# Optimization experiments

Hardware: AMD Instinct MI355X
Metric: run time of the kernel (lower is better)

Reference implementation:

```python
import jax, jax.numpy as jnp
import numpy as np

B, S, D, H, DK, DV = 4, 2048, 512, 8, 64, 64


def setup_inputs() -> dict:
    key0 = jax.random.key(0)
    ks = jax.random.split(key0, 11)
    w = 0.02
    return {
        "query": jax.random.normal(ks[0], (B, S, D), dtype=jnp.float32),
        "key": jax.random.normal(ks[1], (B, S, D), dtype=jnp.float32),
        "value": jax.random.normal(ks[2], (B, S, D), dtype=jnp.float32),
        "Wq": jax.random.normal(ks[3], (D, DK), dtype=jnp.float32) * w,
        "bq": jnp.zeros((DK,), dtype=jnp.float32),
        "Wk": jax.random.normal(ks[4], (D, DK), dtype=jnp.float32) * w,
        "bk": jnp.zeros((DK,), dtype=jnp.float32),
        "Wv": jax.random.normal(ks[5], (D, DV), dtype=jnp.float32) * w,
        "bv": jnp.zeros((DV,), dtype=jnp.float32),
        "Wo": jax.random.normal(ks[6], (H * DV, D), dtype=jnp.float32) * w,
        "bo": jnp.zeros((D,), dtype=jnp.float32),
    }


def reference(query, key, value, Wq, bq, Wk, bk, Wv, bv, Wo, bo):
    # NOTE: original module applies the SAME Dense layers to every head
    # (q_list = [self.query(query) for _ in range(heads)]), so all H heads
    # are mathematically identical -> compute one head and replicate.
    # NOTE: V is projected from `key`, not `value` (faithful to source bug).
    q = query @ Wq + bq          # [B, S, DK]
    k = key @ Wk + bk            # [B, S, DK]
    v = key @ Wv + bv            # [B, S, DV]
    scale = np.sqrt(DK).astype(np.float32)
    scores = jnp.einsum("bqd,bkd->bqk", q, k) / scale  # [B, S, S]
    # masked_mha=True and training=True -> causal mask, fill -1e19
    causal = jnp.triu(jnp.ones((S, S), dtype=scores.dtype), 1)
    scores = scores + causal * jnp.asarray(-1e19, scores.dtype)
    attn = jax.nn.softmax(scores, axis=-1)              # [B, S, S]
    o = jnp.einsum("bqk,bkv->bqv", attn, v)             # [B, S, DV]
    # concat of H identical heads along last axis == tile
    concat = jnp.tile(o, (1, 1, H))                     # [B, S, H*DV]
    return concat @ Wo + bo                             # [B, S, D]
```

## Files before the change

kernel.cpp:

```cpp
#include <hip/hip_runtime.h>
#include <hip/hip_bf16.h>


#define BB 4
#define SS 2048
#define BS (BB*SS)
#define MSHIFT 8.0f

typedef __bf16 v8bf __attribute__((ext_vector_type(8)));
typedef __bf16 v4bf __attribute__((ext_vector_type(4)));
typedef float  v4f  __attribute__((ext_vector_type(4)));

__device__ inline v8bf cvt8(float4 f0, float4 f1) {
    v8bf r;
    r[0] = (__bf16)f0.x; r[1] = (__bf16)f0.y; r[2] = (__bf16)f0.z; r[3] = (__bf16)f0.w;
    r[4] = (__bf16)f1.x; r[5] = (__bf16)f1.y; r[6] = (__bf16)f1.z; r[7] = (__bf16)f1.w;
    return r;
}

__global__ __launch_bounds__(512) void prep_kernel(
    const float* __restrict__ Wq, const float* __restrict__ bq,
    const float* __restrict__ Wk, const float* __restrict__ bk,
    const float* __restrict__ Wv, const float* __restrict__ bv,
    const float* __restrict__ Wo,
    __bf16* __restrict__ Wt, float* __restrict__ bs,
    __bf16* __restrict__ WoEt)
{
    const int t = threadIdx.x, y = blockIdx.y;
    const int idx = blockIdx.x * 512 + t;
    if (y < 3) {
        const float* W  = (y == 0) ? Wq : (y == 1) ? Wk : Wv;
        const float* bb = (y == 0) ? bq : (y == 1) ? bk : bv;
        const float s = (y == 0) ? (0.125f * 1.44269504088896340736f) : 1.0f;
        int c = idx & 63, k = idx >> 6;
        Wt[y * 32768 + c * 512 + k] = (__bf16)(W[k * 64 + c] * s);
        if (blockIdx.x == 0 && t < 64) bs[y * 64 + t] = bb[t] * s;
    } else {
        int d = idx & 511, k = idx >> 9;
        float sum = 0.f;
#pragma unroll
        for (int h = 0; h < 8; h++) sum += Wo[(size_t)(h * 64 + k) * 512 + d];
        WoEt[d * 64 + k] = (__bf16)sum;
    }
}

__global__ __launch_bounds__(256) void proj_kernel(
    const float* __restrict__ query, const float* __restrict__ key,
    const __bf16* __restrict__ Wt, const float* __restrict__ bs,
    __bf16* __restrict__ Qp, __bf16* __restrict__ Kp, __bf16* __restrict__ Vt)
{
    const int t = threadIdx.x;
    const int gw = (blockIdx.x * 256 + t) >> 6;
    const int lane = t & 63, lq = lane & 15, quad = lane >> 4;
    const int kind = gw >> 11;
    const int rr  = gw & 2047;
    const int rows = (rr >> 2) * 16;
    const int cb   = (rr & 3) * 16;
    const float* arow = ((kind == 0) ? query : key) + (size_t)(rows + lq) * 512;

    if (kind == 0) {
        const __bf16* W = Wt + (cb + lq) * 512;
        const float bb = bs[cb + lq];
        v4f acc = {bb, bb, bb, bb};
#pragma unroll 4
        for (int k0 = 0; k0 < 512; k0 += 32) {
            float4 f0 = *(const float4*)(arow + k0 + quad * 8);
            float4 f1 = *(const float4*)(arow + k0 + quad * 8 + 4);
            v8bf a = cvt8(f0, f1);
            v8bf b = *(const v8bf*)(W + k0 + quad * 8);
            acc = __builtin_amdgcn_mfma_f32_16x16x32_bf16(a, b, acc, 0, 0, 0);
        }
#pragma unroll
        for (int r = 0; r < 4; r++)
            Qp[(size_t)(rows + quad * 4 + r) * 64 + cb + lq] = (__bf16)acc[r];
    } else {
        const __bf16* Wk_ = Wt + 32768  + (cb + lq) * 512;
        const __bf16* Wv_ = Wt + 65536  + (cb + lq) * 512;
        const float bk_ = bs[64 + cb + lq], bv_ = bs[128 + cb + lq];
        v4f ak = {bk_, bk_, bk_, bk_}, av = {bv_, bv_, bv_, bv_};
#pragma unroll 4
        for (int k0 = 0; k0 < 512; k0 += 32) {
            float4 f0 = *(const float4*)(arow + k0 + quad * 8);
            float4 f1 = *(const float4*)(arow + k0 + quad * 8 + 4);
            v8bf a  = cvt8(f0, f1);
            v8bf b0 = *(const v8bf*)(Wk_ + k0 + quad * 8);
            v8bf b1 = *(const v8bf*)(Wv_ + k0 + quad * 8);
            ak = __builtin_amdgcn_mfma_f32_16x16x32_bf16(a, b0, ak, 0, 0, 0);
            av = __builtin_amdgcn_mfma_f32_16x16x32_bf16(a, b1, av, 0, 0, 0);
        }
#pragma unroll
        for (int r = 0; r < 4; r++)
            Kp[(size_t)(rows + quad * 4 + r) * 64 + cb + lq] = (__bf16)ak[r];
        v4bf o4; o4[0] = (__bf16)av[0]; o4[1] = (__bf16)av[1];
        o4[2] = (__bf16)av[2]; o4[3] = (__bf16)av[3];
        *(v4bf*)&Vt[(size_t)(cb + lq) * BS + rows + quad * 4] = o4;
    }
}

__global__ __launch_bounds__(256) void attn_kernel(
    const __bf16* __restrict__ Qp,
    const __bf16* __restrict__ Kp,
    const __bf16* __restrict__ Vt,
    __bf16* __restrict__ Opart,
    float* __restrict__ lpart,
    int nch)
{
    __shared__ __bf16 Ks[64][72];
    __shared__ __bf16 Vs[64][72];
    __shared__ __bf16 Ps[4][16][72];

    const int t    = threadIdx.x;
    const int lane = t & 63;
    const int w    = t >> 6;
    const int b    = blockIdx.x & 3;
    const int qt   = 31 - (blockIdx.x >> 2);
    const int c    = blockIdx.y;
    const int qbase = qt * 64;
    const int L    = qbase + 64;
    const int cs   = ((L + nch * 64 - 1) / (nch * 64)) * 64;
    const int klo  = c * cs;
    const int khi  = min(klo + cs, L);
    const size_t bbase = (size_t)b * SS;

    const int lq   = lane & 15;
    const int quad = lane >> 4;
    const int qrow_w = qbase + w * 16;
    const int wmax   = qrow_w + 15;

    const size_t qoff = (bbase + qrow_w + lq) * 64;
    v8bf qa0 = *(const v8bf*)(Qp + qoff + quad * 8);
    v8bf qa1 = *(const v8bf*)(Qp + qoff + 32 + quad * 8);

    v8bf ones;
#pragma unroll
    for (int i = 0; i < 8; i++) ones[i] = (__bf16)1.0f;

    v4f o[4] = {};
    v4f lacc = {};

    const int ky0 = t >> 3,         dd0 = (t & 7) * 8;
    const int ky1 = (t + 256) >> 3, dd1 = dd0;

    v8bf kpre0, kpre1, vpre0, vpre1;
    if (klo < khi) {
        kpre0 = *(const v8bf*)(Kp + (bbase + klo + ky0) * 64 + dd0);
        kpre1 = *(const v8bf*)(Kp + (bbase + klo + ky1) * 64 + dd1);
        vpre0 = *(const v8bf*)(Vt + (size_t)ky0 * BS + bbase + klo + dd0);
        vpre1 = *(const v8bf*)(Vt + (size_t)ky1 * BS + bbase + klo + dd1);
    }

    for (int kb = klo; kb < khi; kb += 64) {
        __syncthreads();
        *(v8bf*)&Ks[ky0][dd0] = kpre0;
        *(v8bf*)&Ks[ky1][dd1] = kpre1;
        *(v8bf*)&Vs[ky0][dd0] = vpre0;
        *(v8bf*)&Vs[ky1][dd1] = vpre1;
        if (kb + 64 < khi) {
            kpre0 = *(const v8bf*)(Kp + (bbase + kb + 64 + ky0) * 64 + dd0);
            kpre1 = *(const v8bf*)(Kp + (bbase + kb + 64 + ky1) * 64 + dd1);
            vpre0 = *(const v8bf*)(Vt + (size_t)ky0 * BS + bbase + kb + 64 + dd0);
            vpre1 = *(const v8bf*)(Vt + (size_t)ky1 * BS + bbase + kb + 64 + dd1);
        }
        __syncthreads();
        if (kb > wmax) continue;

        v4f s[4];
#pragma unroll
        for (int n = 0; n < 4; n++) {
            v8bf ka  = *(const v8bf*)&Ks[n * 16 + lq][quad * 8];
            v8bf kb2 = *(const v8bf*)&Ks[n * 16 + lq][32 + quad * 8];
            v4f z = {0.f, 0.f, 0.f, 0.f};
            z    = __builtin_amdgcn_mfma_f32_16x16x32_bf16(qa0, ka,  z, 0, 0, 0);
            s[n] = __builtin_amdgcn_mfma_f32_16x16x32_bf16(qa1, kb2, z, 0, 0, 0);
        }

        const int row0 = qrow_w + quad * 4;
        const int col0 = kb + lq;
#pragma unroll
        for (int n = 0; n < 4; n++)
#pragma unroll
            for (int r = 0; r < 4; r++) {
                float e = exp2f(s[n][r] - MSHIFT);
                e = (col0 + n * 16 > row0 + r) ? 0.f : e;
                Ps[w][quad * 4 + r][n * 16 + lq] = (__bf16)e;
            }
        v8bf pa0 = *(const v8bf*)&Ps[w][lq][quad * 8];
        v8bf pa1 = *(const v8bf*)&Ps[w][lq][32 + quad * 8];

        lacc = __builtin_amdgcn_mfma_f32_16x16x32_bf16(pa0, ones, lacc, 0, 0, 0);
        lacc = __builtin_amdgcn_mfma_f32_16x16x32_bf16(pa1, ones, lacc, 0, 0, 0);

#pragma unroll
        for (int vt = 0; vt < 4; vt++) {
            v8bf vb0 = *(const v8bf*)&Vs[vt * 16 + lq][quad * 8];
            v8bf vb1 = *(const v8bf*)&Vs[vt * 16 + lq][32 + quad * 8];
            o[vt] = __builtin_amdgcn_mfma_f32_16x16x32_bf16(pa0, vb0, o[vt], 0, 0, 0);
            o[vt] = __builtin_amdgcn_mfma_f32_16x16x32_bf16(pa1, vb1, o[vt], 0, 0, 0);
        }
    }

#pragma unroll
    for (int vt = 0; vt < 4; vt++)
#pragma unroll
        for (int r = 0; r < 4; r++) {
            int qrow = qrow_w + quad * 4 + r;
            Opart[((size_t)c * BS + bbase + qrow) * 64 + vt * 16 + lq] = (__bf16)o[vt][r];
        }
    if (lq < 4) {
        int qrow = qrow_w + quad * 4 + lq;
        lpart[(size_t)c * BS + bbase + qrow] = lacc[lq];
    }
}

__global__ __launch_bounds__(256) void outmerge_kernel(
    const __bf16* __restrict__ Opart, const float* __restrict__ lpart,
    const __bf16* __restrict__ WoEt, const float* __restrict__ bo,
    float* __restrict__ out, int nch)
{
    __shared__ __bf16 Os[16][72];
    const int t = threadIdx.x;
    const int rows0 = blockIdx.x * 16;
    {
        int row = t >> 4, d0 = (t & 15) * 4;
        float den = 0.f;
        for (int c = 0; c < nch; c++) den += lpart[(size_t)c * BS + rows0 + row];
        const float inv = 1.f / den;
        float a0 = 0.f, a1 = 0.f, a2 = 0.f, a3 = 0.f;
        for (int c = 0; c < nch; c++) {
            v4bf v = *(const v4bf*)&Opart[((size_t)c * BS + rows0 + row) * 64 + d0];
            a0 += (float)v[0]; a1 += (float)v[1]; a2 += (float)v[2]; a3 += (float)v[3];
        }
        Os[row][d0] = (__bf16)(a0 * inv); Os[row][d0 + 1] = (__bf16)(a1 * inv);
        Os[row][d0 + 2] = (__bf16)(a2 * inv); Os[row][d0 + 3] = (__bf16)(a3 * inv);
    }
    __syncthreads();

    const int lane = t & 63, lq = lane & 15, quad = lane >> 4;
    const int w = t >> 6;
    v8bf a0 = *(const v8bf*)&Os[lq][quad * 8];
    v8bf a1 = *(const v8bf*)&Os[lq][32 + quad * 8];
#pragma unroll
    for (int i = 0; i < 8; i++) {
        const int cb = (w * 8 + i) * 16;
        v8bf b0 = *(const v8bf*)(WoEt + (size_t)(cb + lq) * 64 + quad * 8);
        v8bf b1 = *(const v8bf*)(WoEt + (size_t)(cb + lq) * 64 + 32 + quad * 8);
        const float bb = bo[cb + lq];
        v4f acc = {bb, bb, bb, bb};
        acc = __builtin_amdgcn_mfma_f32_16x16x32_bf16(a0, b0, acc, 0, 0, 0);
        acc = __builtin_amdgcn_mfma_f32_16x16x32_bf16(a1, b1, acc, 0, 0, 0);
#pragma unroll
        for (int r = 0; r < 4; r++)
            out[(size_t)(rows0 + quad * 4 + r) * 512 + cb + lq] = acc[r];
    }
}

extern "C" void kernel_launch(void* const* d_in, const int* in_sizes, int n_in,
                              void* d_out, int out_size, void* d_ws, size_t ws_size,
                              hipStream_t stream) {
    const float* query = (const float*)d_in[0];
    const float* key   = (const float*)d_in[1];
    const float* Wq = (const float*)d_in[3];
    const float* bq = (const float*)d_in[4];
    const float* Wk = (const float*)d_in[5];
    const float* bk = (const float*)d_in[6];
    const float* Wv = (const float*)d_in[7];
    const float* bv = (const float*)d_in[8];
    const float* Wo = (const float*)d_in[9];
    const float* bo = (const float*)d_in[10];
    float* out = (float*)d_out;

    const int nch = (ws_size >= (size_t)12 * 1024 * 1024) ? 8 : 4;

    char* p = (char*)d_ws;
    __bf16* Qp    = (__bf16*)p; p += (size_t)BS * 64 * 2;
    __bf16* Kp    = (__bf16*)p; p += (size_t)BS * 64 * 2;
    __bf16* Vtg   = (__bf16*)p; p += (size_t)BS * 64 * 2;
    __bf16* Opart = (__bf16*)p; p += (size_t)nch * BS * 64 * 2;
    float* lpart = (float*)p;  p += (size_t)nch * BS * 4;
    __bf16* WoEt = (__bf16*)p; p += (size_t)64 * 512 * 2;
    __bf16* Wt   = (__bf16*)p; p += (size_t)3 * 64 * 512 * 2;
    float* bs    = (float*)p;  p += (size_t)3 * 64 * 4;

    prep_kernel<<<dim3(64, 4), 512, 0, stream>>>(Wq, bq, Wk, bk, Wv, bv, Wo, Wt, bs, WoEt);
    proj_kernel<<<1024, 256, 0, stream>>>(query, key, Wt, bs, Qp, Kp, Vtg);
    attn_kernel<<<dim3(128, nch), 256, 0, stream>>>(Qp, Kp, Vtg, Opart, lpart, nch);
    outmerge_kernel<<<512, 256, 0, stream>>>(Opart, lpart, WoEt, bo, out, nch);
}
```

Baseline: 150.2 us.

## Fuse all four kernels into one cooperative persistent kernel with grid syncs

Merges weight prep, QKV projection, chunked causal attention and output merge/projection into a single cooperative launch of 512 blocks, using grid-wide syncs between phases. Each block handles two attention chunks in sequence, and NCH is now fixed at 8. The aim is to remove three kernel launch gaps and the tail idle time between them. In exchange it adds grid.sync overhead, caps occupancy at 2 blocks per CU, and drops the fallback that used fewer chunks when the workspace is small.

Measured after the change: 463.4 us. 3.09x slower.

```diff
diff --git a/kernel.cpp b/kernel.cpp
--- a/kernel.cpp
+++ b/kernel.cpp
@@ -1,11 +1,16 @@
 #include <hip/hip_runtime.h>
 #include <hip/hip_bf16.h>
+#include <hip/hip_cooperative_groups.h>
+
+namespace cg = cooperative_groups;
 
 
 #define BB 4
 #define SS 2048
 #define BS (BB*SS)
+#define NCH 8
 #define MSHIFT 8.0f
+#define QSCALE (0.125f * 1.44269504088896340736f)
 
 typedef __bf16 v8bf __attribute__((ext_vector_type(8)));
 typedef __bf16 v4bf __attribute__((ext_vector_type(4)));
@@ -18,239 +23,250 @@
     return r;
 }
 
-__global__ __launch_bounds__(512) void prep_kernel(
+__global__ __launch_bounds__(256, 2) void fused_kernel(
+    const float* __restrict__ query, const float* __restrict__ key,
     const float* __restrict__ Wq, const float* __restrict__ bq,
     const float* __restrict__ Wk, const float* __restrict__ bk,
     const float* __restrict__ Wv, const float* __restrict__ bv,
-    const float* __restrict__ Wo,
-    __bf16* __restrict__ Wt, float* __restrict__ bs,
+    const float* __restrict__ Wo, const float* __restrict__ bo,
+    float* __restrict__ out,
+    __bf16* __restrict__ Qp,
+    __bf16* __restrict__ Kp,
+    __bf16* __restrict__ Vt,
+    __bf16* __restrict__ Opart,
+    float* __restrict__ lpart,
+    __bf16* __restrict__ Wt,
+    float* __restrict__ bs,
     __bf16* __restrict__ WoEt)
 {
-    const int t = threadIdx.x, y = blockIdx.y;
-    const int idx = blockIdx.x * 512 + t;
-    if (y < 3) {
-        const float* W  = (y == 0) ? Wq : (y == 1) ? Wk : Wv;
-        const float* bb = (y == 0) ? bq : (y == 1) ? bk : bv;
-        const float s = (y == 0) ? (0.125f * 1.44269504088896340736f) : 1.0f;
-        int c = idx & 63, k = idx >> 6;
-        Wt[y * 32768 + c * 512 + k] = (__bf16)(W[k * 64 + c] * s);
-        if (blockIdx.x == 0 && t < 64) bs[y * 64 + t] = bb[t] * s;
-    } else {
-        int d = idx & 511, k = idx >> 9;
-        float sum = 0.f;
-#pragma unroll
-        for (int h = 0; h < 8; h++) sum += Wo[(size_t)(h * 64 + k) * 512 + d];
-        WoEt[d * 64 + k] = (__bf16)sum;
-    }
-}
-
-__global__ __launch_bounds__(256) void proj_kernel(
-    const float* __restrict__ query, const float* __restrict__ key,
-    const __bf16* __restrict__ Wt, const float* __restrict__ bs,
-    __bf16* __restrict__ Qp, __bf16* __restrict__ Kp, __bf16* __restrict__ Vt)
-{
-    const int t = threadIdx.x;
-    const int gw = (blockIdx.x * 256 + t) >> 6;
-    const int lane = t & 63, lq = lane & 15, quad = lane >> 4;
-    const int kind = gw >> 11;
-    const int rr  = gw & 2047;
-    const int rows = (rr >> 2) * 16;
-    const int cb   = (rr & 3) * 16;
-    const float* arow = ((kind == 0) ? query : key) + (size_t)(rows + lq) * 512;
-
-    if (kind == 0) {
-        const __bf16* W = Wt + (cb + lq) * 512;
-        const float bb = bs[cb + lq];
-        v4f acc = {bb, bb, bb, bb};
-#pragma unroll 4
-        for (int k0 = 0; k0 < 512; k0 += 32) {
-            float4 f0 = *(const float4*)(arow + k0 + quad * 8);
-            float4 f1 = *(const float4*)(arow + k0 + quad * 8 + 4);
-            v8bf a = cvt8(f0, f1);
-            v8bf b = *(const v8bf*)(W + k0 + quad * 8);
-            acc = __builtin_amdgcn_mfma_f32_16x16x32_bf16(a, b, acc, 0, 0, 0);
-        }
-#pragma unroll
-        for (int r = 0; r < 4; r++)
-            Qp[(size_t)(rows + quad * 4 + r) * 64 + cb + lq] = (__bf16)acc[r];
-    } else {
-        const __bf16* Wk_ = Wt + 32768  + (cb + lq) * 512;
-        const __bf16* Wv_ = Wt + 65536  + (cb + lq) * 512;
-        const float bk_ = bs[64 + cb + lq], bv_ = bs[128 + cb + lq];
-        v4f ak = {bk_, bk_, bk_, bk_}, av = {bv_, bv_, bv_, bv_};
-#pragma unroll 4
-        for (int k0 = 0; k0 < 512; k0 += 32) {
-            float4 f0 = *(const float4*)(arow + k0 + quad * 8);
-            float4 f1 = *(const float4*)(arow + k0 + quad * 8 + 4);
-            v8bf a  = cvt8(f0, f1);
-            v8bf b0 = *(const v8bf*)(Wk_ + k0 + quad * 8);
-            v8bf b1 = *(const v8bf*)(Wv_ + k0 + quad * 8);
-            ak = __builtin_amdgcn_mfma_f32_16x16x32_bf16(a, b0, ak, 0, 0, 0);
-            av = __builtin_amdgcn_mfma_f32_16x16x32_bf16(a, b1, av, 0, 0, 0);
-        }
-#pragma unroll
-        for (int r = 0; r < 4; r++)
-            Kp[(size_t)(rows + quad * 4 + r) * 64 + cb + lq] = (__bf16)ak[r];
-        v4bf o4; o4[0] = (__bf16)av[0]; o4[1] = (__bf16)av[1];
-        o4[2] = (__bf16)av[2]; o4[3] = (__bf16)av[3];
-        *(v4bf*)&Vt[(size_t)(cb + lq) * BS + rows + quad * 4] = o4;
-    }
-}
-
-__global__ __launch_bounds__(256) void attn_kernel(
-    const __bf16* __restrict__ Qp,
-    const __bf16* __restrict__ Kp,
-    const __bf16* __restrict__ Vt,
-    __bf16* __restrict__ Opart,
-    float* __restrict__ lpart,
-    int nch)
-{
-    __shared__ __bf16 Ks[64][72];
-    __shared__ __bf16 Vs[64][72];
-    __shared__ __bf16 Ps[4][16][72];
+    cg::grid_group grid = cg::this_grid();
+    __shared__ __align__(16) unsigned char smem[27648];
 
     const int t    = threadIdx.x;
+    const int bi   = blockIdx.x;
     const int lane = t & 63;
-    const int w    = t >> 6;
-    const int b    = blockIdx.x & 3;
-    const int qt   = 31 - (blockIdx.x >> 2);
-    const int c    = blockIdx.y;
-    const int qbase = qt * 64;
-    const int L    = qbase + 64;
-    const int cs   = ((L + nch * 64 - 1) / (nch * 64)) * 64;
-    const int klo  = c * cs;
-    const int khi  = min(klo + cs, L);
-    const size_t bbase = (size_t)b * SS;
-
     const int lq   = lane & 15;
     const int quad = lane >> 4;
-    const int qrow_w = qbase + w * 16;
-    const int wmax   = qrow_w + 15;
-
-    const size_t qoff = (bbase + qrow_w + lq) * 64;
-    v8bf qa0 = *(const v8bf*)(Qp + qoff + quad * 8);
-    v8bf qa1 = *(const v8bf*)(Qp + qoff + 32 + quad * 8);
-
-    v8bf ones;
-#pragma unroll
-    for (int i = 0; i < 8; i++) ones[i] = (__bf16)1.0f;
-
-    v4f o[4] = {};
-    v4f lacc = {};
-
-    const int ky0 = t >> 3,         dd0 = (t & 7) * 8;
-    const int ky1 = (t + 256) >> 3, dd1 = dd0;
-
-    v8bf kpre0, kpre1, vpre0, vpre1;
-    if (klo < khi) {
-        kpre0 = *(const v8bf*)(Kp + (bbase + klo + ky0) * 64 + dd0);
-        kpre1 = *(const v8bf*)(Kp + (bbase + klo + ky1) * 64 + dd1);
-        vpre0 = *(const v8bf*)(Vt + (size_t)ky0 * BS + bbase + klo + dd0);
-        vpre1 = *(const v8bf*)(Vt + (size_t)ky1 * BS + bbase + klo + dd1);
+    const int w    = t >> 6;
+
+    {
+        int tid = bi * 256 + t;
+        for (int i = tid; i < 131264; i += 131072) {
+            if (i < 98304) {
+                int y = i >> 15, r = i & 32767;
+                int c = r & 63, k = r >> 6;
+                const float* W = (y == 0) ? Wq : (y == 1) ? Wk : Wv;
+                float s = (y == 0) ? QSCALE : 1.0f;
+                Wt[y * 32768 + c * 512 + k] = (__bf16)(W[k * 64 + c] * s);
+            } else if (i < 131072) {
+                int r = i - 98304, d = r & 511, k = r >> 9;
+                float sum = 0.f;
+#pragma unroll
+                for (int h = 0; h < 8; h++) sum += Wo[(size_t)(h * 64 + k) * 512 + d];
+                WoEt[d * 64 + k] = (__bf16)sum;
+            } else {
+                int r = i - 131072, y = r >> 6, c = r & 63;
+                const float* bb = (y == 0) ? bq : (y == 1) ? bk : bv;
+                float s = (y == 0) ? QSCALE : 1.0f;
+                bs[y * 64 + c] = bb[c] * s;
+            }
+        }
     }
-
-    for (int kb = klo; kb < khi; kb += 64) {
+    __threadfence();
+    grid.sync();
+
+    {
+        const int gwv  = bi * 4 + w;
+        const int rows = (gwv >> 2) * 16;
+        const int cb   = (gwv & 3) * 16;
+        {
+            const float* arow = query + (size_t)(rows + lq) * 512;
+            const __bf16* W = Wt + (cb + lq) * 512;
+            const float bb = bs[cb + lq];
+            v4f acc = {bb, bb, bb, bb};
+#pragma unroll 4
+            for (int k0 = 0; k0 < 512; k0 += 32) {
+                float4 f0 = *(const float4*)(arow + k0 + quad * 8);
+                float4 f1 = *(const float4*)(arow + k0 + quad * 8 + 4);
+                v8bf a = cvt8(f0, f1);
+                v8bf bfr = *(const v8bf*)(W + k0 + quad * 8);
+                acc = __builtin_amdgcn_mfma_f32_16x16x32_bf16(a, bfr, acc, 0, 0, 0);
+            }
+#pragma unroll
+            for (int r = 0; r < 4; r++)
+                Qp[(size_t)(rows + quad * 4 + r) * 64 + cb + lq] = (__bf16)acc[r];
+        }
+        {
+            const float* arow = key + (size_t)(rows + lq) * 512;
+            const __bf16* Wk_ = Wt + 32768 + (cb + lq) * 512;
+            const __bf16* Wv_ = Wt + 65536 + (cb + lq) * 512;
+            const float bk_ = bs[64 + cb + lq], bv_ = bs[128 + cb + lq];
+            v4f ak = {bk_, bk_, bk_, bk_}, av = {bv_, bv_, bv_, bv_};
+#pragma unroll 4
+            for (int k0 = 0; k0 < 512; k0 += 32) {
+                float4 f0 = *(const float4*)(arow + k0 + quad * 8);
+                float4 f1 = *(const float4*)(arow + k0 + quad * 8 + 4);
+                v8bf a  = cvt8(f0, f1);
+                v8bf b0 = *(const v8bf*)(Wk_ + k0 + quad * 8);
+                v8bf b1 = *(const v8bf*)(Wv_ + k0 + quad * 8);
+                ak = __builtin_amdgcn_mfma_f32_16x16x32_bf16(a, b0, ak, 0, 0, 0);
+                av = __builtin_amdgcn_mfma_f32_16x16x32_bf16(a, b1, av, 0, 0, 0);
+            }
+#pragma unroll
+            for (int r = 0; r < 4; r++)
+                Kp[(size_t)(rows + quad * 4 + r) * 64 + cb + lq] = (__bf16)ak[r];
+            v4bf o4; o4[0] = (__bf16)av[0]; o4[1] = (__bf16)av[1];
+            o4[2] = (__bf16)av[2]; o4[3] = (__bf16)av[3];
+            *(v4bf*)&Vt[(size_t)(cb + lq) * BS + rows + quad * 4] = o4;
+        }
+    }
+    __threadfence();
+    grid.sync();
+
+    {
+        __bf16 (*Ks)[72] = (__bf16(*)[72])smem;
+        __bf16 (*Vs)[72] = (__bf16(*)[72])(smem + 9216);
+        __bf16 (*Ps)[72] = (__bf16(*)[72])(smem + 18432 + w * 2304);
+
+        const int x  = bi & 127;
+        const int c0 = bi >> 7;
+        const int b  = x & 3;
+        const int qt = 31 - (x >> 2);
+        const int qbase = qt * 64;
+        const int L  = qbase + 64;
+        const int cs = ((L + NCH * 64 - 1) / (NCH * 64)) * 64;
+        const size_t bbase = (size_t)b * SS;
+        const int qrow_w = qbase + w * 16;
+        const int wmax   = qrow_w + 15;
+
+        const size_t qoff = (bbase + qrow_w + lq) * 64;
+        v8bf qa0 = *(const v8bf*)(Qp + qoff + quad * 8);
+        v8bf qa1 = *(const v8bf*)(Qp + qoff + 32 + quad * 8);
+
+        v8bf ones;
+#pragma unroll
+        for (int i = 0; i < 8; i++) ones[i] = (__bf16)1.0f;
+
+        const int ky0 = t >> 3, dd0 = (t & 7) * 8;
+        const int ky1 = ky0 + 32;
+
+#pragma unroll 1
+        for (int cc = 0; cc < 2; cc++) {
+            const int c   = c0 + cc * 4;
+            const int klo = c * cs;
+            const int khi = min(klo + cs, L);
+            v4f o[4] = {};
+            v4f lacc = {};
+
+            v8bf kpre0, kpre1, vpre0, vpre1;
+            if (klo < khi) {
+                kpre0 = *(const v8bf*)(Kp + (bbase + klo + ky0) * 64 + dd0);
+                kpre1 = *(const v8bf*)(Kp + (bbase + klo + ky1) * 64 + dd0);
+                vpre0 = *(const v8bf*)(Vt + (size_t)ky0 * BS + bbase + klo + dd0);
+                vpre1 = *(const v8bf*)(Vt + (size_t)ky1 * BS + bbase + klo + dd0);
+            }
+
+            for (int kb = klo; kb < khi; kb += 64) {
+                __syncthreads();
+                *(v8bf*)&Ks[ky0][dd0] = kpre0;
+                *(v8bf*)&Ks[ky1][dd0] = kpre1;
+                *(v8bf*)&Vs[ky0][dd0] = vpre0;
+                *(v8bf*)&Vs[ky1][dd0] = vpre1;
+                if (kb + 64 < khi) {
+                    kpre0 = *(const v8bf*)(Kp + (bbase + kb + 64 + ky0) * 64 + dd0);
+                    kpre1 = *(const v8bf*)(Kp + (bbase + kb + 64 + ky1) * 64 + dd0);
+                    vpre0 = *(const v8bf*)(Vt + (size_t)ky0 * BS + bbase + kb + 64 + dd0);
+                    vpre1 = *(const v8bf*)(Vt + (size_t)ky1 * BS + bbase + kb + 64 + dd0);
+                }
+                __syncthreads();
+                if (kb > wmax) continue;
+
+                v4f s[4];
+#pragma unroll
+                for (int n = 0; n < 4; n++) {
+                    v8bf ka  = *(const v8bf*)&Ks[n * 16 + lq][quad * 8];
+                    v8bf kb2 = *(const v8bf*)&Ks[n * 16 + lq][32 + quad * 8];
+                    v4f z = {0.f, 0.f, 0.f, 0.f};
+                    z    = __builtin_amdgcn_mfma_f32_16x16x32_bf16(qa0, ka,  z, 0, 0, 0);
+                    s[n] = __builtin_amdgcn_mfma_f32_16x16x32_bf16(qa1, kb2, z, 0, 0, 0);
+                }
+
+                const int row0 = qrow_w + quad * 4;
+                const int col0 = kb + lq;
+#pragma unroll
+                for (int n = 0; n < 4; n++)
+#pragma unroll
+                    for (int r = 0; r < 4; r++) {
+                        float e = exp2f(s[n][r] - MSHIFT);
+                        e = (col0 + n * 16 > row0 + r) ? 0.f : e;
+                        Ps[quad * 4 + r][n * 16 + lq] = (__bf16)e;
+                    }
+                v8bf pa0 = *(const v8bf*)&Ps[lq][quad * 8];
+                v8bf pa1 = *(const v8bf*)&Ps[lq][32 + quad * 8];
+
+                lacc = __builtin_amdgcn_mfma_f32_16x16x32_bf16(pa0, ones, lacc, 0, 0, 0);
+                lacc = __builtin_amdgcn_mfma_f32_16x16x32_bf16(pa1, ones, lacc, 0, 0, 0);
+
+#pragma unroll
+                for (int vt = 0; vt < 4; vt++) {
+                    v8bf vb0 = *(const v8bf*)&Vs[vt * 16 + lq][quad * 8];
+                    v8bf vb1 = *(const v8bf*)&Vs[vt * 16 + lq][32 + quad * 8];
+                    o[vt] = __builtin_amdgcn_mfma_f32_16x16x32_bf16(pa0, vb0, o[vt], 0, 0, 0);
+                    o[vt] = __builtin_amdgcn_mfma_f32_16x16x32_bf16(pa1, vb1, o[vt], 0, 0, 0);
+                }
+            }
+
+#pragma unroll
+            for (int vt = 0; vt < 4; vt++)
+#pragma unroll
+                for (int r = 0; r < 4; r++) {
+                    int qrow = qrow_w + quad * 4 + r;
+                    Opart[((size_t)c * BS + bbase + qrow) * 64 + vt * 16 + lq] = (__bf16)o[vt][r];
+                }
+            if (lq < 4) {
+                int qrow = qrow_w + quad * 4 + lq;
+                lpart[(size_t)c * BS + bbase + qrow] = lacc[lq];
+            }
+        }
+    }
+    __threadfence();
+    grid.sync();
+
+    {
+        __bf16 (*Os)[72] = (__bf16(*)[72])smem;
+        const int rows0 = bi * 16;
+        {
+            int row = t >> 4, d0 = (t & 15) * 4;
+            float den = 0.f;
+#pragma unroll
+            for (int c = 0; c < NCH; c++) den += lpart[(size_t)c * BS + rows0 + row];
+            const float inv = 1.f / den;
+            float a0 = 0.f, a1 = 0.f, a2 = 0.f, a3 = 0.f;
+#pragma unroll
+            for (int c = 0; c < NCH; c++) {
+                v4bf v = *(const v4bf*)&Opart[((size_t)c * BS + rows0 + row) * 64 + d0];
+                a0 += (float)v[0]; a1 += (float)v[1]; a2 += (float)v[2]; a3 += (float)v[3];
+            }
+            Os[row][d0] = (__bf16)(a0 * inv); Os[row][d0 + 1] = (__bf16)(a1 * inv);
+            Os[row][d0 + 2] = (__bf16)(a2 * inv); Os[row][d0 + 3] = (__bf16)(a3 * inv);
+        }
         __syncthreads();
-        *(v8bf*)&Ks[ky0][dd0] = kpre0;
-        *(v8bf*)&Ks[ky1][dd1] = kpre1;
-        *(v8bf*)&Vs[ky0][dd0] = vpre0;
-        *(v8bf*)&Vs[ky1][dd1] = vpre1;
-        if (kb + 64 < khi) {
-            kpre0 = *(const v8bf*)(Kp + (bbase + kb + 64 + ky0) * 64 + dd0);
-            kpre1 = *(const v8bf*)(Kp + (bbase + kb + 64 + ky1) * 64 + dd1);
-            vpre0 = *(const v8bf*)(Vt + (size_t)ky0 * BS + bbase + kb + 64 + dd0);
-            vpre1 = *(const v8bf*)(Vt + (size_t)ky1 * BS + bbase + kb + 64 + dd1);
-        }
-        __syncthreads();
-        if (kb > wmax) continue;
-
-        v4f s[4];
-#pragma unroll
-        for (int n = 0; n < 4; n++) {
-            v8bf ka  = *(const v8bf*)&Ks[n * 16 + lq][quad * 8];
-            v8bf kb2 = *(const v8bf*)&Ks[n * 16 + lq][32 + quad * 8];
-            v4f z = {0.f, 0.f, 0.f, 0.f};
-            z    = __builtin_amdgcn_mfma_f32_16x16x32_bf16(qa0, ka,  z, 0, 0, 0);
-            s[n] = __builtin_amdgcn_mfma_f32_16x16x32_bf16(qa1, kb2, z, 0, 0, 0);
-        }
-
-        const int row0 = qrow_w + quad * 4;
-        const int col0 = kb + lq;
-#pragma unroll
-        for (int n = 0; n < 4; n++)
-#pragma unroll
-            for (int r = 0; r < 4; r++) {
-                float e = exp2f(s[n][r] - MSHIFT);
-                e = (col0 + n * 16 > row0 + r) ? 0.f : e;
-                Ps[w][quad * 4 + r][n * 16 + lq] = (__bf16)e;
-            }
-        v8bf pa0 = *(const v8bf*)&Ps[w][lq][quad * 8];
-        v8bf pa1 = *(const v8bf*)&Ps[w][lq][32 + quad * 8];
-
-        lacc = __builtin_amdgcn_mfma_f32_16x16x32_bf16(pa0, ones, lacc, 0, 0, 0);
-        lacc = __builtin_amdgcn_mfma_f32_16x16x32_bf16(pa1, ones, lacc, 0, 0, 0);
-
-#pragma unroll
-        for (int vt = 0; vt < 4; vt++) {
-            v8bf vb0 = *(const v8bf*)&Vs[vt * 16 + lq][quad * 8];
-            v8bf vb1 = *(const v8bf*)&Vs[vt * 16 + lq][32 + quad * 8];
-            o[vt] = __builtin_amdgcn_mfma_f32_16x16x32_bf16(pa0, vb0, o[vt], 0, 0, 0);
-            o[vt] = __builtin_amdgcn_mfma_f32_16x16x32_bf16(pa1, vb1, o[vt], 0, 0, 0);
-        }
-    }
-
-#pragma unroll
-    for (int vt = 0; vt < 4; vt++)
-#pragma unroll
-        for (int r = 0; r < 4; r++) {
-            int qrow = qrow_w + quad * 4 + r;
-            Opart[((size_t)c * BS + bbase + qrow) * 64 + vt * 16 + lq] = (__bf16)o[vt][r];
-        }
-    if (lq < 4) {
-        int qrow = qrow_w + quad * 4 + lq;
-        lpart[(size_t)c * BS + bbase + qrow] = lacc[lq];
-    }
-}
-
-__global__ __launch_bounds__(256) void outmerge_kernel(
-    const __bf16* __restrict__ Opart, const float* __restrict__ lpart,
-    const __bf16* __restrict__ WoEt, const float* __restrict__ bo,
-    float* __restrict__ out, int nch)
-{
-    __shared__ __bf16 Os[16][72];
-    const int t = threadIdx.x;
-    const int rows0 = blockIdx.x * 16;
-    {
-        int row = t >> 4, d0 = (t & 15) * 4;
-        float den = 0.f;
-        for (int c = 0; c < nch; c++) den += lpart[(size_t)c * BS + rows0 + row];
-        const float inv = 1.f / den;
-        float a0 = 0.f, a1 = 0.f, a2 = 0.f, a3 = 0.f;
-        for (int c = 0; c < nch; c++) {
-            v4bf v = *(const v4bf*)&Opart[((size_t)c * BS + rows0 + row) * 64 + d0];
-            a0 += (float)v[0]; a1 += (float)v[1]; a2 += (float)v[2]; a3 += (float)v[3];
-        }
-        Os[row][d0] = (__bf16)(a0 * inv); Os[row][d0 + 1] = (__bf16)(a1 * inv);
-        Os[row][d0 + 2] = (__bf16)(a2 * inv); Os[row][d0 + 3] = (__bf16)(a3 * inv);
-    }
-    __syncthreads();
-
-    const int lane = t & 63, lq = lane & 15, quad = lane >> 4;
-    const int w = t >> 6;
-    v8bf a0 = *(const v8bf*)&Os[lq][quad * 8];
-    v8bf a1 = *(const v8bf*)&Os[lq][32 + quad * 8];
-#pragma unroll
-    for (int i = 0; i < 8; i++) {
-        const int cb = (w * 8 + i) * 16;
-        v8bf b0 = *(const v8bf*)(WoEt + (size_t)(cb + lq) * 64 + quad * 8);
-        v8bf b1 = *(const v8bf*)(WoEt + (size_t)(cb + lq) * 64 + 32 + quad * 8);
-        const float bb = bo[cb + lq];
-        v4f acc = {bb, bb, bb, bb};
-        acc = __builtin_amdgcn_mfma_f32_16x16x32_bf16(a0, b0, acc, 0, 0, 0);
-        acc = __builtin_amdgcn_mfma_f32_16x16x32_bf16(a1, b1, acc, 0, 0, 0);
-#pragma unroll
-        for (int r = 0; r < 4; r++)
-            out[(size_t)(rows0 + quad * 4 + r) * 512 + cb + lq] = acc[r];
+
+        v8bf a0 = *(const v8bf*)&Os[lq][quad * 8];
+        v8bf a1 = *(const v8bf*)&Os[lq][32 + quad * 8];
+#pragma unroll
+        for (int i = 0; i < 8; i++) {
+            const int cb = (w * 8 + i) * 16;
+            v8bf b0 = *(const v8bf*)(WoEt + (size_t)(cb + lq) * 64 + quad * 8);
+            v8bf b1 = *(const v8bf*)(WoEt + (size_t)(cb + lq) * 64 + 32 + quad * 8);
+            const float bb = bo[cb + lq];
+            v4f acc = {bb, bb, bb, bb};
+            acc = __builtin_amdgcn_mfma_f32_16x16x32_bf16(a0, b0, acc, 0, 0, 0);
+            acc = __builtin_amdgcn_mfma_f32_16x16x32_bf16(a1, b1, acc, 0, 0, 0);
+#pragma unroll
+            for (int r = 0; r < 4; r++)
+                out[(size_t)(rows0 + quad * 4 + r) * 512 + cb + lq] = acc[r];
+        }
     }
 }
 
@@ -269,20 +285,22 @@
     const float* bo = (const float*)d_in[10];
     float* out = (float*)d_out;
 
-    const int nch = (ws_size >= (size_t)12 * 1024 * 1024) ? 8 : 4;
-
     char* p = (char*)d_ws;
     __bf16* Qp    = (__bf16*)p; p += (size_t)BS * 64 * 2;
     __bf16* Kp    = (__bf16*)p; p += (size_t)BS * 64 * 2;
     __bf16* Vtg   = (__bf16*)p; p += (size_t)BS * 64 * 2;
-    __bf16* Opart = (__bf16*)p; p += (size_t)nch * BS * 64 * 2;
-    float* lpart = (float*)p;  p += (size_t)nch * BS * 4;
-    __bf16* WoEt = (__bf16*)p; p += (size_t)64 * 512 * 2;
-    __bf16* Wt   = (__bf16*)p; p += (size_t)3 * 64 * 512 * 2;
-    float* bs    = (float*)p;  p += (size_t)3 * 64 * 4;
-
-    prep_kernel<<<dim3(64, 4), 512, 0, stream>>>(Wq, bq, Wk, bk, Wv, bv, Wo, Wt, bs, WoEt);
-    proj_kernel<<<1024, 256, 0, stream>>>(query, key, Wt, bs, Qp, Kp, Vtg);
-    attn_kernel<<<dim3(128, nch), 256, 0, stream>>>(Qp, Kp, Vtg, Opart, lpart, nch);
-    outmerge_kernel<<<512, 256, 0, stream>>>(Opart, lpart, WoEt, bo, out, nch);
+    __bf16* Opart = (__bf16*)p; p += (size_t)NCH * BS * 64 * 2;
+    float* lpart  = (float*)p;  p += (size_t)NCH * BS * 4;
+    __bf16* WoEt  = (__bf16*)p; p += (size_t)64 * 512 * 2;
+    __bf16* Wt    = (__bf16*)p; p += (size_t)3 * 64 * 512 * 2;
+    float* bsv    = (float*)p;  p += (size_t)3 * 64 * 4;
+
+    void* args[] = {
+        (void*)&query, (void*)&key, (void*)&Wq, (void*)&bq, (void*)&Wk,
+        (void*)&bk, (void*)&Wv, (void*)&bv, (void*)&Wo, (void*)&bo,
+        (void*)&out, (void*)&Qp, (void*)&Kp, (void*)&Vtg, (void*)&Opart,
+        (void*)&lpart, (void*)&Wt, (void*)&bsv, (void*)&WoEt
+    };
+    hipLaunchCooperativeKernel((const void*)fused_kernel, dim3(512), dim3(256),
+                               args, 0, stream);
 }
```
